# Performance work log

Hardware: AMD Instinct MI355X
Metric: run time of the kernel (lower is better)

Reference implementation:

```python
import jax, jax.numpy as jnp
import numpy as np

B = 16384
F = 128   # num_features
H = 128   # hidden_dim
E = 32    # embedding_dim


def setup_inputs() -> dict:
    key = jax.random.key(0)
    k_x, k_w1, k_b1, k_w2, k_b2 = jax.random.split(key, 5)
    # Per-feature params stacked along feature axis.
    # Layer 1: Linear(1 -> H): weight [F, H] (in_dim==1 squeezed), bias [F, H]
    # Layer 2: Linear(H -> E): weight [F, H, E], bias [F, E]
    # Torch default init: U(-1/sqrt(fan_in), 1/sqrt(fan_in))
    w1 = jax.random.uniform(k_w1, (F, H), jnp.float32, -1.0, 1.0)          # fan_in=1
    b1 = jax.random.uniform(k_b1, (F, H), jnp.float32, -1.0, 1.0)
    bound2 = 1.0 / np.sqrt(H)
    w2 = jax.random.uniform(k_w2, (F, H, E), jnp.float32, -bound2, bound2)
    b2 = jax.random.uniform(k_b2, (F, E), jnp.float32, -bound2, bound2)
    x = jax.random.normal(k_x, (B, F), jnp.float32)
    return {"x": x, "w1": w1, "b1": b1, "w2": w2, "b2": b2}


def reference(x, w1, b1, w2, b2):
    # Fused over features: broadcast-mul replaces K=1 matmuls,
    # single batched GEMM replaces per-feature second Linear.
    h = jax.nn.relu(x[:, :, None] * w1[None] + b1[None])   # [B, F, H]
    out = jnp.einsum('bfh,fhe->bfe', h, w2) + b2[None]      # [B, F, E]
    return out.reshape(x.shape[0], F * E)                   # concat along last dim
```

## Files before the change

### kernel.cpp

```cpp
#include <hip/hip_runtime.h>
#include <math.h>

#define B_N 16384
#define F_N 128
#define H_N 128
#define E_N 32
#define ROWS (H_N + 1)

__global__ __launch_bounds__(128) void build_tables(
    const float* __restrict__ w1, const float* __restrict__ b1,
    const float* __restrict__ w2, const float* __restrict__ b2,
    float* __restrict__ ts_out, float* __restrict__ tab)
{
    __shared__ float w1s[H_N], b1s[H_N], ts[H_N];
    __shared__ int   hidx[H_N];
    __shared__ float w2s[H_N * E_N];
    __shared__ float dA[H_N * E_N];
    __shared__ float dC[H_N * E_N];
    __shared__ float baseA[4 * E_N], baseC[4 * E_N];

    const int f   = blockIdx.x;
    const int tid = threadIdx.x;

    float w1v = w1[f * H_N + tid];
    float b1v = b1[f * H_N + tid];
    w1s[tid] = w1v;
    b1s[tid] = b1v;
    ts[tid]   = (w1v != 0.0f) ? (-b1v / w1v) : INFINITY;
    hidx[tid] = tid;

    {
        const float4* src = (const float4*)(w2 + (size_t)f * H_N * E_N);
        float4*       dst = (float4*)w2s;
        #pragma unroll
        for (int it = 0; it < 8; ++it) dst[it * 128 + tid] = src[it * 128 + tid];
    }
    __syncthreads();

    for (int k = 2; k <= H_N; k <<= 1) {
        for (int j = k >> 1; j > 0; j >>= 1) {
            int ixj = tid ^ j;
            if (ixj > tid) {
                float a = ts[tid], bv = ts[ixj];
                bool up = ((tid & k) == 0);
                bool sw = up ? (a > bv) : (a < bv);
                if (sw) {
                    int ia = hidx[tid];
                    ts[tid] = bv; ts[ixj] = a;
                    hidx[tid] = hidx[ixj]; hidx[ixj] = ia;
                }
            }
            __syncthreads();
        }
    }

    ts_out[f * H_N + tid] = ts[tid];

    const int e = tid & 31;
    const int g = tid >> 5;

    #pragma unroll 4
    for (int jj = 0; jj < 32; ++jj) {
        int   j   = g * 32 + jj;
        int   p   = hidx[j];
        float w1h = w1s[p], b1h = b1s[p];
        float w2v = w2s[p * E_N + e];
        float s   = (w1h > 0.f) ? 1.f : ((w1h < 0.f) ? -1.f : 0.f);
        dA[j * E_N + e] = s * w1h * w2v;
        dC[j * E_N + e] = s * b1h * w2v;
    }
    {
        float pA = 0.f, pC = 0.f;
        #pragma unroll 4
        for (int hh = 0; hh < 32; ++hh) {
            int   h   = g * 32 + hh;
            float w1h = w1s[h], b1h = b1s[h];
            float w2v = w2s[h * E_N + e];
            if (w1h < 0.f) {
                pA = fmaf(w1h, w2v, pA);
                pC = fmaf(b1h, w2v, pC);
            } else if (w1h == 0.f && b1h > 0.f) {
                pC = fmaf(b1h, w2v, pC);
            }
        }
        baseA[g * E_N + e] = pA;
        baseC[g * E_N + e] = pC;
    }
    __syncthreads();

    if (tid < E_N) {
        float accA = baseA[e] + baseA[E_N + e] + baseA[2 * E_N + e] + baseA[3 * E_N + e];
        float accC = baseC[e] + baseC[E_N + e] + baseC[2 * E_N + e] + baseC[3 * E_N + e];
        accC += b2[f * E_N + e];
        const size_t base = (size_t)f * ROWS * 64;
        tab[base + e]        = accA;
        tab[base + 32 + e]   = accC;
        for (int j = 0; j < H_N; ++j) {
            accA += dA[j * E_N + e];
            accC += dC[j * E_N + e];
            tab[base + (size_t)(j + 1) * 64 + e]      = accA;
            tab[base + (size_t)(j + 1) * 64 + 32 + e] = accC;
        }
    }
}

#define FH 32
#define NB 64
#define CH 8

__global__ __launch_bounds__(256) void apply_tables(
    const float* __restrict__ x, const float* __restrict__ ts,
    const float* __restrict__ tab, float* __restrict__ out)
{
    __shared__ float lds_t[FH * ROWS];
    __shared__ float xs[NB * FH];

    const int tid = threadIdx.x;
    const int b0  = blockIdx.x * NB;
    const int f0  = blockIdx.y * FH;

    {
        const float4* src = (const float4*)(ts + (size_t)f0 * H_N);
        #pragma unroll
        for (int it = 0; it < (FH * H_N / 4) / 256; ++it) {
            int    vi  = it * 256 + tid;
            float4 v   = src[vi];
            int    idx = vi * 4;
            int    fl  = idx >> 7;
            int    j   = idx & 127;
            float* dst = &lds_t[fl * ROWS + j];
            dst[0] = v.x; dst[1] = v.y; dst[2] = v.z; dst[3] = v.w;
        }
    }
    {
        #pragma unroll
        for (int it = 0; it < (NB * FH / 4) / 256; ++it) {
            int vi = it * 256 + tid;
            int bl = vi >> 3;
            int fq = (vi & 7) * 4;
            float4 v = *(const float4*)(x + (size_t)(b0 + bl) * F_N + f0 + fq);
            *(float4*)(&xs[bl * FH + fq]) = v;
        }
    }
    __syncthreads();

    const int fl = tid >> 3;
    const int eq = tid & 7;
    const int fg = f0 + fl;
    const float* tloc     = &lds_t[fl * ROWS];
    const size_t tab_base = (size_t)fg * ROWS * 64 + eq * 4;
    const size_t out_base = (size_t)b0 * (F_N * E_N) + (size_t)fg * E_N + eq * 4;

    for (int c = 0; c < NB / CH; ++c) {
        float xv[CH];
        int   lo[CH], hi[CH];
        #pragma unroll
        for (int j = 0; j < CH; ++j) {
            xv[j] = xs[(c * CH + j) * FH + fl];
            lo[j] = 0;
            hi[j] = H_N;
        }
        #pragma unroll
        for (int s = 0; s < 7; ++s) {
            #pragma unroll
            for (int j = 0; j < CH; ++j) {
                int  mid = (lo[j] + hi[j]) >> 1;
                bool lt  = tloc[mid] < xv[j];
                lo[j] = lt ? mid + 1 : lo[j];
                hi[j] = lt ? hi[j] : mid;
            }
        }
        #pragma unroll
        for (int j = 0; j < CH; ++j) {
            const float* row = tab + tab_base + (size_t)lo[j] * 64;
            float4 a4 = *(const float4*)(row);
            float4 c4 = *(const float4*)(row + 32);
            float  xj = xv[j];
            float4 o;
            o.x = fmaf(xj, a4.x, c4.x);
            o.y = fmaf(xj, a4.y, c4.y);
            o.z = fmaf(xj, a4.z, c4.z);
            o.w = fmaf(xj, a4.w, c4.w);
            *(float4*)(out + out_base + (size_t)(c * CH + j) * (F_N * E_N)) = o;
        }
    }
}

__global__ __launch_bounds__(256) void direct_kernel(
    const float* __restrict__ x, const float* __restrict__ w1,
    const float* __restrict__ b1, const float* __restrict__ w2,
    const float* __restrict__ b2, float* __restrict__ out)
{
    __shared__ float w1s[H_N], b1s[H_N], b2s[E_N];
    __shared__ float w2s[H_N * E_N];
    const int f   = blockIdx.y;
    const int tid = threadIdx.x;
    if (tid < H_N) { w1s[tid] = w1[f * H_N + tid]; b1s[tid] = b1[f * H_N + tid]; }
    for (int i = tid; i < H_N * E_N; i += 256) w2s[i] = w2[(size_t)f * H_N * E_N + i];
    if (tid < E_N) b2s[tid] = b2[f * E_N + tid];
    __syncthreads();

    const int b  = blockIdx.x * 256 + tid;
    float xv = x[(size_t)b * F_N + f];
    float acc[E_N];
    #pragma unroll
    for (int e = 0; e < E_N; ++e) acc[e] = b2s[e];
    for (int h = 0; h < H_N; ++h) {
        float hv = fmaxf(fmaf(xv, w1s[h], b1s[h]), 0.f);
        #pragma unroll
        for (int e = 0; e < E_N; ++e) acc[e] = fmaf(hv, w2s[h * E_N + e], acc[e]);
    }
    float* op = out + (size_t)b * (F_N * E_N) + (size_t)f * E_N;
    #pragma unroll
    for (int e = 0; e < E_N; e += 4)
        *(float4*)(op + e) = make_float4(acc[e], acc[e + 1], acc[e + 2], acc[e + 3]);
}

extern "C" void kernel_launch(void* const* d_in, const int* in_sizes, int n_in,
                              void* d_out, int out_size, void* d_ws, size_t ws_size,
                              hipStream_t stream) {
    const float* x  = (const float*)d_in[0];
    const float* w1 = (const float*)d_in[1];
    const float* b1 = (const float*)d_in[2];
    const float* w2 = (const float*)d_in[3];
    const float* b2 = (const float*)d_in[4];
    float* out = (float*)d_out;

    const size_t n_ts  = (size_t)F_N * H_N;
    const size_t n_tab = (size_t)F_N * ROWS * 64;
    const size_t need  = (n_ts + n_tab) * sizeof(float);

    if (ws_size >= need) {
        float* ts  = (float*)d_ws;
        float* tab = ts + n_ts;
        build_tables<<<dim3(F_N), dim3(128), 0, stream>>>(w1, b1, w2, b2, ts, tab);
        apply_tables<<<dim3(B_N / NB, F_N / FH), dim3(256), 0, stream>>>(x, ts, tab, out);
    } else {
        direct_kernel<<<dim3(B_N / 256, F_N), dim3(256), 0, stream>>>(x, w1, b1, w2, b2, out);
    }
}
```

Before: 339.0 us.

## Parallelize table prefix sums and split binary search from nontemporal output writes

```diff
diff --git a/kernel.cpp b/kernel.cpp
--- a/kernel.cpp
+++ b/kernel.cpp
@@ -6,6 +6,8 @@
 #define H_N 128
 #define E_N 32
 #define ROWS (H_N + 1)
+
+typedef float f4v __attribute__((ext_vector_type(4)));
 
 __global__ __launch_bounds__(128) void build_tables(
     const float* __restrict__ w1, const float* __restrict__ b1,
@@ -18,6 +20,7 @@
     __shared__ float dA[H_N * E_N];
     __shared__ float dC[H_N * E_N];
     __shared__ float baseA[4 * E_N], baseC[4 * E_N];
+    __shared__ float gtA[4 * E_N], gtC[4 * E_N];
 
     const int f   = blockIdx.x;
     const int tid = threadIdx.x;
@@ -86,43 +89,62 @@
         baseA[g * E_N + e] = pA;
         baseC[g * E_N + e] = pC;
     }
-    __syncthreads();
-
-    if (tid < E_N) {
-        float accA = baseA[e] + baseA[E_N + e] + baseA[2 * E_N + e] + baseA[3 * E_N + e];
-        float accC = baseC[e] + baseC[E_N + e] + baseC[2 * E_N + e] + baseC[3 * E_N + e];
-        accC += b2[f * E_N + e];
-        const size_t base = (size_t)f * ROWS * 64;
-        tab[base + e]        = accA;
-        tab[base + 32 + e]   = accC;
-        for (int j = 0; j < H_N; ++j) {
-            accA += dA[j * E_N + e];
-            accC += dC[j * E_N + e];
-            tab[base + (size_t)(j + 1) * 64 + e]      = accA;
-            tab[base + (size_t)(j + 1) * 64 + 32 + e] = accC;
-        }
+
+    {
+        float aA = 0.f, aC = 0.f;
+        for (int jj = 0; jj < 32; ++jj) {
+            int idx = (g * 32 + jj) * E_N + e;
+            aA += dA[idx]; dA[idx] = aA;
+            aC += dC[idx]; dC[idx] = aC;
+        }
+        gtA[g * E_N + e] = aA;
+        gtC[g * E_N + e] = aC;
+    }
+    __syncthreads();
+
+    float offA = baseA[e] + baseA[E_N + e] + baseA[2 * E_N + e] + baseA[3 * E_N + e];
+    float offC = baseC[e] + baseC[E_N + e] + baseC[2 * E_N + e] + baseC[3 * E_N + e]
+               + b2[f * E_N + e];
+    for (int gg = 0; gg < g; ++gg) {
+        offA += gtA[gg * E_N + e];
+        offC += gtC[gg * E_N + e];
+    }
+
+    const size_t base = (size_t)f * ROWS * 64;
+    if (g == 0) {
+        tab[base + e]      = offA;
+        tab[base + 32 + e] = offC;
+    }
+    #pragma unroll 4
+    for (int jj = 0; jj < 32; ++jj) {
+        int j = g * 32 + jj;
+        tab[base + (size_t)(j + 1) * 64 + e]      = offA + dA[j * E_N + e];
+        tab[base + (size_t)(j + 1) * 64 + 32 + e] = offC + dC[j * E_N + e];
     }
 }
 
 #define FH 32
 #define NB 64
-#define CH 8
-
-__global__ __launch_bounds__(256) void apply_tables(
+
+__global__ __launch_bounds__(256, 4) void apply_tables(
     const float* __restrict__ x, const float* __restrict__ ts,
     const float* __restrict__ tab, float* __restrict__ out)
 {
     __shared__ float lds_t[FH * ROWS];
     __shared__ float xs[NB * FH];
+    __shared__ int   los[NB * FH];
 
     const int tid = threadIdx.x;
-    const int b0  = blockIdx.x * NB;
-    const int f0  = blockIdx.y * FH;
+
+    const unsigned bid  = blockIdx.x;
+    const unsigned work = (bid & 7u) * 128u + (bid >> 3);
+    const int b0 = (int)(work & 255u) * NB;
+    const int f0 = (int)(work >> 8)  * FH;
 
     {
         const float4* src = (const float4*)(ts + (size_t)f0 * H_N);
         #pragma unroll
-        for (int it = 0; it < (FH * H_N / 4) / 256; ++it) {
+        for (int it = 0; it < 4; ++it) {
             int    vi  = it * 256 + tid;
             float4 v   = src[vi];
             int    idx = vi * 4;
@@ -134,7 +156,7 @@
     }
     {
         #pragma unroll
-        for (int it = 0; it < (NB * FH / 4) / 256; ++it) {
+        for (int it = 0; it < 2; ++it) {
             int vi = it * 256 + tid;
             int bl = vi >> 3;
             int fq = (vi & 7) * 4;
@@ -144,26 +166,21 @@
     }
     __syncthreads();
 
-    const int fl = tid >> 3;
-    const int eq = tid & 7;
-    const int fg = f0 + fl;
-    const float* tloc     = &lds_t[fl * ROWS];
-    const size_t tab_base = (size_t)fg * ROWS * 64 + eq * 4;
-    const size_t out_base = (size_t)b0 * (F_N * E_N) + (size_t)fg * E_N + eq * 4;
-
-    for (int c = 0; c < NB / CH; ++c) {
-        float xv[CH];
-        int   lo[CH], hi[CH];
-        #pragma unroll
-        for (int j = 0; j < CH; ++j) {
-            xv[j] = xs[(c * CH + j) * FH + fl];
-            lo[j] = 0;
-            hi[j] = H_N;
+    {
+        const int fa = tid & 31;
+        const int rg = tid >> 5;
+        const float* tloc = &lds_t[fa * ROWS];
+        float xv[8];
+        int   lo[8], hi[8];
+        #pragma unroll
+        for (int j = 0; j < 8; ++j) {
+            xv[j] = xs[(rg * 8 + j) * FH + fa];
+            lo[j] = 0; hi[j] = H_N;
         }
         #pragma unroll
         for (int s = 0; s < 7; ++s) {
             #pragma unroll
-            for (int j = 0; j < CH; ++j) {
+            for (int j = 0; j < 8; ++j) {
                 int  mid = (lo[j] + hi[j]) >> 1;
                 bool lt  = tloc[mid] < xv[j];
                 lo[j] = lt ? mid + 1 : lo[j];
@@ -171,18 +188,29 @@
             }
         }
         #pragma unroll
-        for (int j = 0; j < CH; ++j) {
-            const float* row = tab + tab_base + (size_t)lo[j] * 64;
-            float4 a4 = *(const float4*)(row);
-            float4 c4 = *(const float4*)(row + 32);
-            float  xj = xv[j];
-            float4 o;
-            o.x = fmaf(xj, a4.x, c4.x);
-            o.y = fmaf(xj, a4.y, c4.y);
-            o.z = fmaf(xj, a4.z, c4.z);
-            o.w = fmaf(xj, a4.w, c4.w);
-            *(float4*)(out + out_base + (size_t)(c * CH + j) * (F_N * E_N)) = o;
-        }
+        for (int j = 0; j < 8; ++j) los[(rg * 8 + j) * FH + fa] = lo[j];
+    }
+    __syncthreads();
+
+    const int fl = tid >> 3;
+    const int eq = tid & 7;
+    const int fg = f0 + fl;
+    const float* tb = tab + (size_t)fg * ROWS * 64 + eq * 4;
+    float*       op = out + (size_t)b0 * (F_N * E_N) + (size_t)fg * E_N + eq * 4;
+
+    #pragma unroll 4
+    for (int r = 0; r < NB; ++r) {
+        int   lo = los[r * FH + fl];
+        float xv = xs[r * FH + fl];
+        const float* row = tb + (size_t)lo * 64;
+        f4v a4 = *(const f4v*)(row);
+        f4v c4 = *(const f4v*)(row + 32);
+        f4v o;
+        o.x = fmaf(xv, a4.x, c4.x);
+        o.y = fmaf(xv, a4.y, c4.y);
+        o.z = fmaf(xv, a4.z, c4.z);
+        o.w = fmaf(xv, a4.w, c4.w);
+        __builtin_nontemporal_store(o, (f4v*)(op + (size_t)r * (F_N * E_N)));
     }
 }
 
@@ -234,7 +262,7 @@
         float* ts  = (float*)d_ws;
         float* tab = ts + n_ts;
         build_tables<<<dim3(F_N), dim3(128), 0, stream>>>(w1, b1, w2, b2, ts, tab);
-        apply_tables<<<dim3(B_N / NB, F_N / FH), dim3(256), 0, stream>>>(x, ts, tab, out);
+        apply_tables<<<dim3((B_N / NB) * (F_N / FH)), dim3(256), 0, stream>>>(x, ts, tab, out);
     } else {
         direct_kernel<<<dim3(B_N / 256, F_N), dim3(256), 0, stream>>>(x, w1, b1, w2, b2, out);
     }
```

New measurement: 287.7 us. 15.1% less time.
